# Kernel optimization log

Hardware: AMD Instinct MI355X
Metric: run time of the kernel (lower is better)

Reference implementation:

```python
import jax, jax.numpy as jnp
import numpy as np

NEG_SLOPE = 0.2
EPS = 1e-16

N_NODES = 50000
N_EDGES = 800000
IN_DIM = 64
HEADS = 4
HEAD_DIM = 64


def setup_inputs() -> dict:
    key = jax.random.key(0)
    k1, k2, k3, k4, k5 = jax.random.split(key, 5)
    x = jax.random.normal(k1, (N_NODES, IN_DIM), dtype=jnp.float32)
    edge_index = jax.random.randint(k2, (2, N_EDGES), 0, N_NODES, dtype=jnp.int64)
    W = jax.random.normal(k3, (IN_DIM, HEADS * HEAD_DIM), dtype=jnp.float32) * (1.0 / np.sqrt(IN_DIM))
    att_src = jax.random.normal(k4, (HEADS, HEAD_DIM), dtype=jnp.float32) * 0.1
    att_dst = jax.random.normal(k5, (HEADS, HEAD_DIM), dtype=jnp.float32) * 0.1
    bias = jnp.zeros((HEADS * HEAD_DIM,), dtype=jnp.float32)
    return {"x": x, "edge_index": edge_index, "W": W,
            "att_src": att_src, "att_dst": att_dst, "bias": bias}


def reference(x, edge_index, W, att_src, att_dst, bias):
    N = x.shape[0]
    H, D = att_src.shape
    # add self-loops (PyG default add_self_loops=True)
    loop = jnp.arange(N, dtype=edge_index.dtype)
    src = jnp.concatenate([edge_index[0], loop])  # message source j
    dst = jnp.concatenate([edge_index[1], loop])  # message target i

    h = (x @ W).reshape(N, H, D)                 # [N,H,D] per-head projection
    a_src = jnp.einsum('nhd,hd->nh', h, att_src)  # [N,H]
    a_dst = jnp.einsum('nhd,hd->nh', h, att_dst)  # [N,H]

    score = jax.nn.leaky_relu(a_src[src] + a_dst[dst], NEG_SLOPE)  # [E,H]
    # segment softmax over edges grouped by destination node
    m = jax.ops.segment_max(score, dst, num_segments=N)            # [N,H]
    m = jnp.where(jnp.isfinite(m), m, 0.0)
    e = jnp.exp(score - m[dst])                                    # [E,H]
    denom = jax.ops.segment_sum(e, dst, num_segments=N)            # [N,H]
    alpha = e / (denom[dst] + EPS)                                 # [E,H]

    msgs = h[src] * alpha[:, :, None]                              # [E,H,D]
    out = jax.ops.segment_sum(msgs, dst, num_segments=N)           # [N,H,D]
    return out.reshape(N, H * D) + bias
```

## Files before the change

### kernel.cpp

```cpp
#include <hip/hip_runtime.h>

#define N_NODES 50000
#define N_EDGES 800000
#define E_TOT   850000
#define HD      256
#define MAXDEG  64
#define NEG_SLOPE 0.2f
#define EPS 1e-16f

#define NB     392
#define BSHIFT 7
#define CAP    2944
#define ABLK   392
#define EPB    2304

typedef __attribute__((ext_vector_type(8))) short short8;
typedef __attribute__((ext_vector_type(4))) float f32x4;
typedef __attribute__((ext_vector_type(4))) unsigned int uint4v;

__device__ __forceinline__ unsigned short f2bf(float f) {
    union { float f; unsigned int i; } c; c.f = f;
    unsigned int r = 0x7fffu + ((c.i >> 16) & 1u);
    return (unsigned short)((c.i + r) >> 16);
}
__device__ __forceinline__ float bf2f(unsigned short u) {
    union { unsigned int i; float f; } c; c.i = ((unsigned int)u) << 16;
    return c.f;
}
__device__ __forceinline__ short8 pack8(float4 a, float4 b) {
    short8 r;
    r[0] = (short)f2bf(a.x); r[1] = (short)f2bf(a.y);
    r[2] = (short)f2bf(a.z); r[3] = (short)f2bf(a.w);
    r[4] = (short)f2bf(b.x); r[5] = (short)f2bf(b.y);
    r[6] = (short)f2bf(b.z); r[7] = (short)f2bf(b.w);
    return r;
}
__device__ __forceinline__ float lrelu_exp(float v) {
    v = (v < 0.f) ? v * NEG_SLOPE : v;
    return __expf(v);
}

__global__ __launch_bounds__(256) void prep_kernel(
        const float* __restrict__ W, const float* __restrict__ att_src,
        const float* __restrict__ att_dst, float* __restrict__ ws, float* __restrict__ wd,
        int* __restrict__ gcnt) {
    const int t = threadIdx.x, head = t >> 6, k = t & 63;
    gcnt[t] = 0; gcnt[t + 256] = 0;
    const float* wrow = W + k * 256 + head * 64;
    const float* as = att_src + head * 64;
    const float* adv = att_dst + head * 64;
    float s = 0.f, d = 0.f;
#pragma unroll 8
    for (int j = 0; j < 64; ++j) { s += wrow[j] * as[j]; d += wrow[j] * adv[j]; }
    ws[k * 4 + head] = s;
    wd[k * 4 + head] = d;
}

__global__ __launch_bounds__(256) void bin_logit_kernel(
        const float* __restrict__ x,
        const float4* __restrict__ ws4, const float4* __restrict__ wd4,
        const int* __restrict__ eidx,
        int* __restrict__ gcnt, unsigned int* __restrict__ arena,
        float4* __restrict__ a_src4, float4* __restrict__ a_dst4,
        unsigned short* __restrict__ xb) {
    __shared__ int hist[4][NB];
    __shared__ int abase[4][NB];
    const int t = threadIdx.x;
    const int w = t >> 6;
    const int e0 = blockIdx.x * EPB;
    for (int i = t; i < 4 * NB; i += 256) ((int*)hist)[i] = 0;
    __syncthreads();

#pragma unroll
    for (int k = 0; k < EPB / 256; ++k) {
        const int g = e0 + k * 256 + t;
        if (g < E_TOT) {
            const int d = (g < N_EDGES) ? eidx[N_EDGES + g] : g - N_EDGES;
            atomicAdd(&hist[w][d >> BSHIFT], 1);
        }
    }
    __syncthreads();
    for (int i = t; i < NB; i += 256) {
        const int c0 = hist[0][i], c1 = hist[1][i], c2 = hist[2][i], c3 = hist[3][i];
        const int tot = c0 + c1 + c2 + c3;
        const int base = tot ? atomicAdd(&gcnt[i], tot) : 0;
        abase[0][i] = base;
        abase[1][i] = base + c0;
        abase[2][i] = base + c0 + c1;
        abase[3][i] = base + c0 + c1 + c2;
        hist[0][i] = 0; hist[1][i] = 0; hist[2][i] = 0; hist[3][i] = 0;
    }
    __syncthreads();

#pragma unroll
    for (int k = 0; k < EPB / 256; ++k) {
        const int g = e0 + k * 256 + t;
        if (g < E_TOT) {
            int s, d;
            if (g < N_EDGES) { s = eidx[g]; d = eidx[N_EDGES + g]; }
            else             { s = d = g - N_EDGES; }
            const int b = d >> BSHIFT;
            const int pos = abase[w][b] + atomicAdd(&hist[w][b], 1);
            if (pos < CAP)
                arena[b * CAP + pos] =
                    (unsigned int)s | ((unsigned int)(d & 127) << 16);
        }
    }

    const int g = blockIdx.x * 256 + t;
    if (g < N_NODES) {
        const float4* xr = (const float4*)(x + (size_t)g * 64);
        float4 vs = {0.f, 0.f, 0.f, 0.f};
        float4 vd = {0.f, 0.f, 0.f, 0.f};
#pragma unroll 4
        for (int kk = 0; kk < 16; kk += 2) {
            float4 xv0 = xr[kk];
            float4 xv1 = xr[kk + 1];
            *(short8*)&xb[(size_t)g * 64 + kk * 4] = pack8(xv0, xv1);
#pragma unroll
            for (int j = 0; j < 8; ++j) {
                const float4 xv = (j < 4) ? xv0 : xv1;
                const int jj = j & 3;
                const float xj = jj == 0 ? xv.x : jj == 1 ? xv.y : jj == 2 ? xv.z : xv.w;
                const float4 w1 = ws4[(kk + (j >> 2)) * 4 + jj];
                const float4 w2 = wd4[(kk + (j >> 2)) * 4 + jj];
                vs.x += xj * w1.x; vs.y += xj * w1.y; vs.z += xj * w1.z; vs.w += xj * w1.w;
                vd.x += xj * w2.x; vd.y += xj * w2.y; vd.z += xj * w2.z; vd.w += xj * w2.w;
            }
        }
        a_src4[g] = vs;
        a_dst4[g] = vd;
    }
}

__global__ __launch_bounds__(256) void ell_build_kernel(
        const int* __restrict__ gcnt, const unsigned int* __restrict__ arena,
        int* __restrict__ cnt, unsigned short* __restrict__ slotu) {
    __shared__ int lcnt[128];
    const int t = threadIdx.x;
    const int b = blockIdx.x;
    if (t < 128) lcnt[t] = 0;
    __syncthreads();
    int m = gcnt[b]; if (m > CAP) m = CAP;
    const int n0 = b << BSHIFT;
    const unsigned int* ap = arena + (size_t)b * CAP;
    const uint4v* ap4 = (const uint4v*)ap;
    const int m4 = m >> 2;
    for (int i = t; i < m4; i += 256) {
        const uint4v p4 = __builtin_nontemporal_load(ap4 + i);
#pragma unroll
        for (int j = 0; j < 4; ++j) {
            const unsigned int p = p4[j];
            const int dl = p >> 16;
            const int s  = p & 0xFFFFu;
            const int pos = atomicAdd(&lcnt[dl], 1);
            if (pos < MAXDEG) slotu[(size_t)(n0 + dl) * MAXDEG + pos] = (unsigned short)s;
        }
    }
    for (int i = (m4 << 2) + t; i < m; i += 256) {
        const unsigned int p = ap[i];
        const int dl = p >> 16;
        const int s  = p & 0xFFFFu;
        const int pos = atomicAdd(&lcnt[dl], 1);
        if (pos < MAXDEG) slotu[(size_t)(n0 + dl) * MAXDEG + pos] = (unsigned short)s;
    }
    __syncthreads();
    if (t < 128) {
        const int n = n0 + t;
        if (n < N_NODES) cnt[n] = lcnt[t];
    }
}

__global__ __launch_bounds__(256) void aggregate_x_kernel(
        const int* __restrict__ cnt, const unsigned short* __restrict__ slotu,
        const float4* __restrict__ a_src4, const float4* __restrict__ a_dst4,
        const unsigned short* __restrict__ xb, unsigned short* __restrict__ yb) {
    __shared__ int    lsrc[4][64];
    __shared__ float4 lscs[4][64];
    const int w    = threadIdx.x >> 6;
    const int lane = threadIdx.x & 63;
    const int node = blockIdx.x * 4 + w;
    int deg = cnt[node];
    if (deg > MAXDEG) deg = MAXDEG;
    const size_t base = (size_t)node * MAXDEG;
    const float4 ad = a_dst4[node];

    int s = (lane < deg) ? (int)__builtin_nontemporal_load(&slotu[base + lane]) : 0;
    float4 A = a_src4[s];
    float4 sc;
    if (lane < deg) {
        sc.x = lrelu_exp(A.x + ad.x); sc.y = lrelu_exp(A.y + ad.y);
        sc.z = lrelu_exp(A.z + ad.z); sc.w = lrelu_exp(A.w + ad.w);
    } else {
        sc = (float4){0.f, 0.f, 0.f, 0.f};
    }
    lsrc[w][lane] = s;
    lscs[w][lane] = sc;

    float4 ds = sc;
#pragma unroll
    for (int m = 1; m < 64; m <<= 1) {
        ds.x += __shfl_xor(ds.x, m, 64); ds.y += __shfl_xor(ds.y, m, 64);
        ds.z += __shfl_xor(ds.z, m, 64); ds.w += __shfl_xor(ds.w, m, 64);
    }
    float4 inv;
    inv.x = 1.f / (ds.x + EPS); inv.y = 1.f / (ds.y + EPS);
    inv.z = 1.f / (ds.z + EPS); inv.w = 1.f / (ds.w + EPS);

    const int g  = lane >> 4;
    const int dg = lane & 15;
    float acc[4][4];
#pragma unroll
    for (int h = 0; h < 4; ++h)
#pragma unroll
        for (int j = 0; j < 4; ++j) acc[h][j] = 0.f;

    const int nit = (deg + 7) >> 3;
    float4 cA = lscs[w][g], cB = lscs[w][g + 4];
    int sA = lsrc[w][g], sB = lsrc[w][g + 4];
    ushort4 xA = *(const ushort4*)&xb[(size_t)sA * 64 + dg * 4];
    ushort4 xB = *(const ushort4*)&xb[(size_t)sB * 64 + dg * 4];
    for (int it = 0; it < nit; ++it) {
        ushort4 xnA = xA, xnB = xB;
        float4 cnA = cA, cnB = cB;
        if (it + 1 < nit) {
            const int en = (it + 1) * 8 + g;
            const int snA = lsrc[w][en], snB = lsrc[w][en + 4];
            cnA = lscs[w][en]; cnB = lscs[w][en + 4];
            xnA = *(const ushort4*)&xb[(size_t)snA * 64 + dg * 4];
            xnB = *(const ushort4*)&xb[(size_t)snB * 64 + dg * 4];
        }
        const float a0 = bf2f(xA.x), a1 = bf2f(xA.y), a2 = bf2f(xA.z), a3 = bf2f(xA.w);
        acc[0][0] += a0 * cA.x; acc[0][1] += a1 * cA.x; acc[0][2] += a2 * cA.x; acc[0][3] += a3 * cA.x;
        acc[1][0] += a0 * cA.y; acc[1][1] += a1 * cA.y; acc[1][2] += a2 * cA.y; acc[1][3] += a3 * cA.y;
        acc[2][0] += a0 * cA.z; acc[2][1] += a1 * cA.z; acc[2][2] += a2 * cA.z; acc[2][3] += a3 * cA.z;
        acc[3][0] += a0 * cA.w; acc[3][1] += a1 * cA.w; acc[3][2] += a2 * cA.w; acc[3][3] += a3 * cA.w;
        const float b0 = bf2f(xB.x), b1 = bf2f(xB.y), b2 = bf2f(xB.z), b3 = bf2f(xB.w);
        acc[0][0] += b0 * cB.x; acc[0][1] += b1 * cB.x; acc[0][2] += b2 * cB.x; acc[0][3] += b3 * cB.x;
        acc[1][0] += b0 * cB.y; acc[1][1] += b1 * cB.y; acc[1][2] += b2 * cB.y; acc[1][3] += b3 * cB.y;
        acc[2][0] += b0 * cB.z; acc[2][1] += b1 * cB.z; acc[2][2] += b2 * cB.z; acc[2][3] += b3 * cB.z;
        acc[3][0] += b0 * cB.w; acc[3][1] += b1 * cB.w; acc[3][2] += b2 * cB.w; acc[3][3] += b3 * cB.w;
        xA = xnA; xB = xnB; cA = cnA; cB = cnB;
    }

#pragma unroll
    for (int h = 0; h < 4; ++h)
#pragma unroll
        for (int j = 0; j < 4; ++j) {
            acc[h][j] += __shfl_xor(acc[h][j], 16, 64);
            acc[h][j] += __shfl_xor(acc[h][j], 32, 64);
        }

    const float iv = g == 0 ? inv.x : g == 1 ? inv.y : g == 2 ? inv.z : inv.w;
    const float o0 = (g == 0 ? acc[0][0] : g == 1 ? acc[1][0] : g == 2 ? acc[2][0] : acc[3][0]) * iv;
    const float o1 = (g == 0 ? acc[0][1] : g == 1 ? acc[1][1] : g == 2 ? acc[2][1] : acc[3][1]) * iv;
    const float o2 = (g == 0 ? acc[0][2] : g == 1 ? acc[1][2] : g == 2 ? acc[2][2] : acc[3][2]) * iv;
    const float o3 = (g == 0 ? acc[0][3] : g == 1 ? acc[1][3] : g == 2 ? acc[2][3] : acc[3][3]) * iv;
    ushort4 ov;
    ov.x = f2bf(o0); ov.y = f2bf(o1); ov.z = f2bf(o2); ov.w = f2bf(o3);
    *(ushort4*)&yb[(size_t)node * 256 + g * 64 + dg * 4] = ov;
}

__global__ __launch_bounds__(256) void gemm_out_kernel(
        const unsigned short* __restrict__ yb, const float* __restrict__ W,
        const float* __restrict__ bias, float* __restrict__ out) {
    __shared__ __align__(16) unsigned short Wt[256 * 64];
    const int t = threadIdx.x;
    {
        const int c = t;
        for (int kg = 0; kg < 8; ++kg) {
            float4 lo, hi;
            lo.x = W[(kg * 8 + 0) * 256 + c]; lo.y = W[(kg * 8 + 1) * 256 + c];
            lo.z = W[(kg * 8 + 2) * 256 + c]; lo.w = W[(kg * 8 + 3) * 256 + c];
            hi.x = W[(kg * 8 + 4) * 256 + c]; hi.y = W[(kg * 8 + 5) * 256 + c];
            hi.z = W[(kg * 8 + 6) * 256 + c]; hi.w = W[(kg * 8 + 7) * 256 + c];
            *(short8*)&Wt[c * 64 + ((kg ^ (c & 7)) << 3)] = pack8(lo, hi);
        }
    }
    __syncthreads();

    const int wave = t >> 6, lane = t & 63;
    const int q = lane >> 4, mloc = lane & 15;
    const int rowbase = blockIdx.x * 64 + wave * 16;
    int arow = rowbase + mloc;
    if (arow > N_NODES - 1) arow = N_NODES - 1;

    short8 a0[4], a1[4];
#pragma unroll
    for (int h = 0; h < 4; ++h) {
        const unsigned short* yr = yb + (size_t)arow * 256 + h * 64;
        a0[h] = *(const short8*)&yr[q * 8];
        a1[h] = *(const short8*)&yr[32 + q * 8];
    }

    f32x4 acc[16];
#pragma unroll
    for (int n = 0; n < 16; ++n) acc[n] = (f32x4){0.f, 0.f, 0.f, 0.f};
#pragma unroll
    for (int n = 0; n < 16; ++n) {
        const int c = n * 16 + mloc;
        const int h = n >> 2;
        const unsigned short* rowp = &Wt[c * 64];
        short8 b0 = *(const short8*)&rowp[((q    ) ^ (c & 7)) << 3];
        short8 b1 = *(const short8*)&rowp[((4 + q) ^ (c & 7)) << 3];
        acc[n] = __builtin_amdgcn_mfma_f32_16x16x32_bf16(a0[h], b0, acc[n], 0, 0, 0);
        acc[n] = __builtin_amdgcn_mfma_f32_16x16x32_bf16(a1[h], b1, acc[n], 0, 0, 0);
    }

    float bv[16];
#pragma unroll
    for (int n = 0; n < 16; ++n) bv[n] = bias[n * 16 + mloc];

    const int orow = rowbase + q * 4;
#pragma unroll
    for (int r = 0; r < 4; ++r) {
        if (orow + r < N_NODES) {
            float* op = out + (size_t)(orow + r) * 256 + mloc;
#pragma unroll
            for (int n = 0; n < 16; ++n) op[n * 16] = acc[n][r] + bv[n];
        }
    }
}

extern "C" void kernel_launch(void* const* d_in, const int* in_sizes, int n_in,
                              void* d_out, int out_size, void* d_ws, size_t ws_size,
                              hipStream_t stream) {
    const float* x       = (const float*)d_in[0];
    const int*   eidx    = (const int*)  d_in[1];
    const float* W       = (const float*)d_in[2];
    const float* att_src = (const float*)d_in[3];
    const float* att_dst = (const float*)d_in[4];
    const float* bias    = (const float*)d_in[5];
    float* out = (float*)d_out;

    unsigned short* yb = (unsigned short*)d_ws;
    float* a_src = (float*)(yb + (size_t)N_NODES * HD);
    float* a_dst = a_src + N_NODES * 4;
    float* ws    = a_dst + N_NODES * 4;
    float* wd    = ws + 256;
    int*   cnt   = (int*)(wd + 256);
    int*   gcnt  = cnt + N_NODES;
    unsigned int*   arena = (unsigned int*)(gcnt + 512);
    unsigned short* slotu = (unsigned short*)(arena + NB * CAP);
    unsigned short* xb    = slotu + (size_t)N_NODES * MAXDEG;

    prep_kernel<<<1, 256, 0, stream>>>(W, att_src, att_dst, ws, wd, gcnt);
    bin_logit_kernel<<<ABLK, 256, 0, stream>>>(
        x, (const float4*)ws, (const float4*)wd, eidx, gcnt, arena,
        (float4*)a_src, (float4*)a_dst, xb);
    ell_build_kernel<<<NB, 256, 0, stream>>>(gcnt, arena, cnt, slotu);
    aggregate_x_kernel<<<N_NODES / 4, 256, 0, stream>>>(
        cnt, slotu, (const float4*)a_src, (const float4*)a_dst, xb, yb);
    gemm_out_kernel<<<(N_NODES + 63) / 64, 256, 0, stream>>>(yb, W, bias, out);
}
```

Measured before the change: 174.0 us.

## Split bf16 feature matrix into two planes and aggregate each plane separately

Stores the bf16 copy of x as two 32-column planes and launches the aggregation kernel with twice the blocks, each handling one plane, so that the gathered working set per pass is half as large and more likely to stay cache-resident. Each wavefront now covers 8 edges per iteration with 8 lanes per edge, and adds an extra shuffle stage in the reduction. It also drops the explicit software prefetch in the gather loop and the nontemporal loads for arena and slot data. The cost is that slot loads, attention scores and the softmax denominator are computed twice, once per plane.

```diff
diff --git a/kernel.cpp b/kernel.cpp
--- a/kernel.cpp
+++ b/kernel.cpp
@@ -16,7 +16,6 @@
 
 typedef __attribute__((ext_vector_type(8))) short short8;
 typedef __attribute__((ext_vector_type(4))) float f32x4;
-typedef __attribute__((ext_vector_type(4))) unsigned int uint4v;
 
 __device__ __forceinline__ unsigned short f2bf(float f) {
     union { float f; unsigned int i; } c; c.f = f;
@@ -62,7 +61,7 @@
         const int* __restrict__ eidx,
         int* __restrict__ gcnt, unsigned int* __restrict__ arena,
         float4* __restrict__ a_src4, float4* __restrict__ a_dst4,
-        unsigned short* __restrict__ xb) {
+        unsigned short* __restrict__ xb0, unsigned short* __restrict__ xb1) {
     __shared__ int hist[4][NB];
     __shared__ int abase[4][NB];
     const int t = threadIdx.x;
@@ -116,7 +115,9 @@
         for (int kk = 0; kk < 16; kk += 2) {
             float4 xv0 = xr[kk];
             float4 xv1 = xr[kk + 1];
-            *(short8*)&xb[(size_t)g * 64 + kk * 4] = pack8(xv0, xv1);
+            unsigned short* xp = (kk < 8) ? &xb0[(size_t)g * 32 + kk * 4]
+                                          : &xb1[(size_t)g * 32 + (kk - 8) * 4];
+            *(short8*)xp = pack8(xv0, xv1);
 #pragma unroll
             for (int j = 0; j < 8; ++j) {
                 const float4 xv = (j < 4) ? xv0 : xv1;
@@ -144,13 +145,13 @@
     int m = gcnt[b]; if (m > CAP) m = CAP;
     const int n0 = b << BSHIFT;
     const unsigned int* ap = arena + (size_t)b * CAP;
-    const uint4v* ap4 = (const uint4v*)ap;
+    const uint4* ap4 = (const uint4*)ap;
     const int m4 = m >> 2;
     for (int i = t; i < m4; i += 256) {
-        const uint4v p4 = __builtin_nontemporal_load(ap4 + i);
+        const uint4 p4 = ap4[i];
 #pragma unroll
         for (int j = 0; j < 4; ++j) {
-            const unsigned int p = p4[j];
+            const unsigned int p = j == 0 ? p4.x : j == 1 ? p4.y : j == 2 ? p4.z : p4.w;
             const int dl = p >> 16;
             const int s  = p & 0xFFFFu;
             const int pos = atomicAdd(&lcnt[dl], 1);
@@ -171,21 +172,26 @@
     }
 }
 
-__global__ __launch_bounds__(256) void aggregate_x_kernel(
+__global__ __launch_bounds__(256) void aggregate_plane_kernel(
         const int* __restrict__ cnt, const unsigned short* __restrict__ slotu,
         const float4* __restrict__ a_src4, const float4* __restrict__ a_dst4,
-        const unsigned short* __restrict__ xb, unsigned short* __restrict__ yb) {
+        const unsigned short* __restrict__ xb0, const unsigned short* __restrict__ xb1,
+        unsigned short* __restrict__ yb) {
     __shared__ int    lsrc[4][64];
     __shared__ float4 lscs[4][64];
+    const int plane = (blockIdx.x >= (N_NODES / 4)) ? 1 : 0;
+    const int blk   = blockIdx.x - plane * (N_NODES / 4);
+    const unsigned short* xp = plane ? xb1 : xb0;
+    const int pofs = plane << 5;
     const int w    = threadIdx.x >> 6;
     const int lane = threadIdx.x & 63;
-    const int node = blockIdx.x * 4 + w;
+    const int node = blk * 4 + w;
     int deg = cnt[node];
     if (deg > MAXDEG) deg = MAXDEG;
     const size_t base = (size_t)node * MAXDEG;
     const float4 ad = a_dst4[node];
 
-    int s = (lane < deg) ? (int)__builtin_nontemporal_load(&slotu[base + lane]) : 0;
+    int s = (lane < deg) ? (int)slotu[base + lane] : 0;
     float4 A = a_src4[s];
     float4 sc;
     if (lane < deg) {
@@ -207,8 +213,8 @@
     inv.x = 1.f / (ds.x + EPS); inv.y = 1.f / (ds.y + EPS);
     inv.z = 1.f / (ds.z + EPS); inv.w = 1.f / (ds.w + EPS);
 
-    const int g  = lane >> 4;
-    const int dg = lane & 15;
+    const int g  = lane >> 3;
+    const int dg = lane & 7;
     float acc[4][4];
 #pragma unroll
     for (int h = 0; h < 4; ++h)
@@ -216,49 +222,37 @@
         for (int j = 0; j < 4; ++j) acc[h][j] = 0.f;
 
     const int nit = (deg + 7) >> 3;
-    float4 cA = lscs[w][g], cB = lscs[w][g + 4];
-    int sA = lsrc[w][g], sB = lsrc[w][g + 4];
-    ushort4 xA = *(const ushort4*)&xb[(size_t)sA * 64 + dg * 4];
-    ushort4 xB = *(const ushort4*)&xb[(size_t)sB * 64 + dg * 4];
     for (int it = 0; it < nit; ++it) {
-        ushort4 xnA = xA, xnB = xB;
-        float4 cnA = cA, cnB = cB;
-        if (it + 1 < nit) {
-            const int en = (it + 1) * 8 + g;
-            const int snA = lsrc[w][en], snB = lsrc[w][en + 4];
-            cnA = lscs[w][en]; cnB = lscs[w][en + 4];
-            xnA = *(const ushort4*)&xb[(size_t)snA * 64 + dg * 4];
-            xnB = *(const ushort4*)&xb[(size_t)snB * 64 + dg * 4];
-        }
-        const float a0 = bf2f(xA.x), a1 = bf2f(xA.y), a2 = bf2f(xA.z), a3 = bf2f(xA.w);
-        acc[0][0] += a0 * cA.x; acc[0][1] += a1 * cA.x; acc[0][2] += a2 * cA.x; acc[0][3] += a3 * cA.x;
-        acc[1][0] += a0 * cA.y; acc[1][1] += a1 * cA.y; acc[1][2] += a2 * cA.y; acc[1][3] += a3 * cA.y;
-        acc[2][0] += a0 * cA.z; acc[2][1] += a1 * cA.z; acc[2][2] += a2 * cA.z; acc[2][3] += a3 * cA.z;
-        acc[3][0] += a0 * cA.w; acc[3][1] += a1 * cA.w; acc[3][2] += a2 * cA.w; acc[3][3] += a3 * cA.w;
-        const float b0 = bf2f(xB.x), b1 = bf2f(xB.y), b2 = bf2f(xB.z), b3 = bf2f(xB.w);
-        acc[0][0] += b0 * cB.x; acc[0][1] += b1 * cB.x; acc[0][2] += b2 * cB.x; acc[0][3] += b3 * cB.x;
-        acc[1][0] += b0 * cB.y; acc[1][1] += b1 * cB.y; acc[1][2] += b2 * cB.y; acc[1][3] += b3 * cB.y;
-        acc[2][0] += b0 * cB.z; acc[2][1] += b1 * cB.z; acc[2][2] += b2 * cB.z; acc[2][3] += b3 * cB.z;
-        acc[3][0] += b0 * cB.w; acc[3][1] += b1 * cB.w; acc[3][2] += b2 * cB.w; acc[3][3] += b3 * cB.w;
-        xA = xnA; xB = xnB; cA = cnA; cB = cnB;
+        const int e = it * 8 + g;
+        const int se = lsrc[w][e];
+        const float4 ce = lscs[w][e];
+        const ushort4 xv = *(const ushort4*)&xp[(size_t)se * 32 + dg * 4];
+        const float x0 = bf2f(xv.x), x1 = bf2f(xv.y), x2 = bf2f(xv.z), x3 = bf2f(xv.w);
+        acc[0][0] += x0 * ce.x; acc[0][1] += x1 * ce.x; acc[0][2] += x2 * ce.x; acc[0][3] += x3 * ce.x;
+        acc[1][0] += x0 * ce.y; acc[1][1] += x1 * ce.y; acc[1][2] += x2 * ce.y; acc[1][3] += x3 * ce.y;
+        acc[2][0] += x0 * ce.z; acc[2][1] += x1 * ce.z; acc[2][2] += x2 * ce.z; acc[2][3] += x3 * ce.z;
+        acc[3][0] += x0 * ce.w; acc[3][1] += x1 * ce.w; acc[3][2] += x2 * ce.w; acc[3][3] += x3 * ce.w;
     }
 
 #pragma unroll
     for (int h = 0; h < 4; ++h)
 #pragma unroll
         for (int j = 0; j < 4; ++j) {
+            acc[h][j] += __shfl_xor(acc[h][j],  8, 64);
             acc[h][j] += __shfl_xor(acc[h][j], 16, 64);
             acc[h][j] += __shfl_xor(acc[h][j], 32, 64);
         }
 
-    const float iv = g == 0 ? inv.x : g == 1 ? inv.y : g == 2 ? inv.z : inv.w;
-    const float o0 = (g == 0 ? acc[0][0] : g == 1 ? acc[1][0] : g == 2 ? acc[2][0] : acc[3][0]) * iv;
-    const float o1 = (g == 0 ? acc[0][1] : g == 1 ? acc[1][1] : g == 2 ? acc[2][1] : acc[3][1]) * iv;
-    const float o2 = (g == 0 ? acc[0][2] : g == 1 ? acc[1][2] : g == 2 ? acc[2][2] : acc[3][2]) * iv;
-    const float o3 = (g == 0 ? acc[0][3] : g == 1 ? acc[1][3] : g == 2 ? acc[2][3] : acc[3][3]) * iv;
-    ushort4 ov;
-    ov.x = f2bf(o0); ov.y = f2bf(o1); ov.z = f2bf(o2); ov.w = f2bf(o3);
-    *(ushort4*)&yb[(size_t)node * 256 + g * 64 + dg * 4] = ov;
+    if (g < 4) {
+        const float iv = g == 0 ? inv.x : g == 1 ? inv.y : g == 2 ? inv.z : inv.w;
+        const float o0 = (g == 0 ? acc[0][0] : g == 1 ? acc[1][0] : g == 2 ? acc[2][0] : acc[3][0]) * iv;
+        const float o1 = (g == 0 ? acc[0][1] : g == 1 ? acc[1][1] : g == 2 ? acc[2][1] : acc[3][1]) * iv;
+        const float o2 = (g == 0 ? acc[0][2] : g == 1 ? acc[1][2] : g == 2 ? acc[2][2] : acc[3][2]) * iv;
+        const float o3 = (g == 0 ? acc[0][3] : g == 1 ? acc[1][3] : g == 2 ? acc[2][3] : acc[3][3]) * iv;
+        ushort4 ov;
+        ov.x = f2bf(o0); ov.y = f2bf(o1); ov.z = f2bf(o2); ov.w = f2bf(o3);
+        *(ushort4*)&yb[(size_t)node * 256 + g * 64 + pofs + dg * 4] = ov;
+    }
 }
 
 __global__ __launch_bounds__(256) void gemm_out_kernel(
@@ -342,14 +336,15 @@
     int*   gcnt  = cnt + N_NODES;
     unsigned int*   arena = (unsigned int*)(gcnt + 512);
     unsigned short* slotu = (unsigned short*)(arena + NB * CAP);
-    unsigned short* xb    = slotu + (size_t)N_NODES * MAXDEG;
+    unsigned short* xb0   = slotu + (size_t)N_NODES * MAXDEG;
+    unsigned short* xb1   = xb0 + (size_t)N_NODES * 32;
 
     prep_kernel<<<1, 256, 0, stream>>>(W, att_src, att_dst, ws, wd, gcnt);
     bin_logit_kernel<<<ABLK, 256, 0, stream>>>(
         x, (const float4*)ws, (const float4*)wd, eidx, gcnt, arena,
-        (float4*)a_src, (float4*)a_dst, xb);
+        (float4*)a_src, (float4*)a_dst, xb0, xb1);
     ell_build_kernel<<<NB, 256, 0, stream>>>(gcnt, arena, cnt, slotu);
-    aggregate_x_kernel<<<N_NODES / 4, 256, 0, stream>>>(
-        cnt, slotu, (const float4*)a_src, (const float4*)a_dst, xb, yb);
+    aggregate_plane_kernel<<<2 * (N_NODES / 4), 256, 0, stream>>>(
+        cnt, slotu, (const float4*)a_src, (const float4*)a_dst, xb0, xb1, yb);
     gemm_out_kernel<<<(N_NODES + 63) / 64, 256, 0, stream>>>(yb, W, bias, out);
 }
```

Result: slower. 209.4 us (+20.3%).
